# Kernel optimization log

Hardware: AMD Instinct MI355X
Metric: run time of the kernel (lower is better)

The kernel has to match this reference:

```python
import jax, jax.numpy as jnp
import numpy as np

B, N, D_IN, D_HID = 8, 2048, 512, 512

def setup_inputs() -> dict:
    key = jax.random.key(0)
    k1, k2, k3 = jax.random.split(key, 3)
    inp = jax.random.normal(k1, (B, N, D_IN), dtype=jnp.float32)
    # nn.Linear(input_size, hidden_size): weight [hidden, in], bias [hidden]
    W = jax.random.normal(k2, (D_HID, D_IN), dtype=jnp.float32) * (1.0 / np.sqrt(D_IN))
    b = jax.random.normal(k3, (D_HID,), dtype=jnp.float32) * 0.01
    return {"input": inp, "W": W, "b": b}

def reference(input, W, b):
    # x = fc(input): [B, N, D_HID]
    x = jnp.einsum('bnd,hd->bnh', input, W) + b
    # scores = x @ x^T (NO scale factor, matching the original): [B, N, N]
    scores = jnp.einsum('bnh,bmh->bnm', x, x)
    attn = jax.nn.softmax(scores, axis=2)
    # output = attn @ raw input (V = input, not the projection): [B, N, D_IN]
    output = jnp.einsum('bnm,bmd->bnd', attn, input)
    return output
```

## Files before the change

kernel.cpp:

```cpp
#include <hip/hip_runtime.h>
#include <hip/hip_bf16.h>
#include <stdint.h>

typedef short vbf16x8 __attribute__((ext_vector_type(8)));
typedef float vf32x4 __attribute__((ext_vector_type(4)));
typedef unsigned short u16;

__device__ __forceinline__ float bf2f(u16 u) {
  union { unsigned int i; float f; } v; v.i = ((unsigned int)u) << 16; return v.f;
}
__device__ __forceinline__ u16 f2bf(float f) {
  union { float f; unsigned int i; } v; v.f = f;
  return (u16)((v.i + 0x7fffu + ((v.i >> 16) & 1u)) >> 16);
}
__device__ __forceinline__ void gld16(const void* g, void* l) {
  __builtin_amdgcn_global_load_lds((const __attribute__((address_space(1))) void*)g,
                                   (__attribute__((address_space(3))) void*)l, 16, 0, 0);
}
template<int N> __device__ __forceinline__ void wait_vmcnt() {
  asm volatile("s_waitcnt vmcnt(%0)" :: "n"(N) : "memory");
}
__device__ __forceinline__ vbf16x8 ldsv(const u16* p) { return *(const vbf16x8*)p; }

__global__ __launch_bounds__(256) void k_convw(const float* __restrict__ W, u16* __restrict__ Wb) {
  int i = blockIdx.x * 256 + threadIdx.x;
  float4 x = ((const float4*)W)[i];
  ushort4 h;
  h.x = f2bf(x.x); h.y = f2bf(x.y); h.z = f2bf(x.z); h.w = f2bf(x.w);
  ((ushort4*)Wb)[i] = h;
}

__global__ __launch_bounds__(256) void k_prep(const float* __restrict__ in,
                                              u16* __restrict__ Abf, u16* __restrict__ Vt) {
  __shared__ u16 Ts[64][72];
  const int tid = threadIdx.x;
  const int n0 = blockIdx.x * 64, d0 = blockIdx.y * 64, b = blockIdx.z;
  const float* src = in + ((long long)b * 2048 + n0) * 512 + d0;
#pragma unroll
  for (int j = 0; j < 4; ++j) {
    int chunk = tid + 256 * j;
    int r = chunk >> 4, c = (chunk & 15) * 4;
    float4 x = *(const float4*)(src + (long long)r * 512 + c);
    ushort4 h;
    h.x = f2bf(x.x); h.y = f2bf(x.y); h.z = f2bf(x.z); h.w = f2bf(x.w);
    *(ushort4*)(Abf + ((long long)b * 2048 + n0 + r) * 512 + d0 + c) = h;
    Ts[c + 0][r] = h.x; Ts[c + 1][r] = h.y; Ts[c + 2][r] = h.z; Ts[c + 3][r] = h.w;
  }
  __syncthreads();
#pragma unroll
  for (int j = 0; j < 2; ++j) {
    int chunk = tid + 256 * j;
    int dr = chunk >> 3, c8 = (chunk & 7) * 8;
    vbf16x8 w = *(const vbf16x8*)&Ts[dr][c8];
    *(vbf16x8*)(Vt + ((long long)b * 512 + d0 + dr) * 2048 + n0 + c8) = w;
  }
}

__global__ __launch_bounds__(256) void k_rownorm(const u16* __restrict__ X,
                                                 float* __restrict__ D) {
  const int row = blockIdx.x * 4 + (threadIdx.x >> 6);
  const int lane = threadIdx.x & 63;
  vbf16x8 v = *(const vbf16x8*)(X + (long long)row * 512 + lane * 8);
  float s = 0.0f;
#pragma unroll
  for (int j = 0; j < 8; ++j) { float x = bf2f((u16)v[j]); s = fmaf(x, x, s); }
  for (int o = 1; o < 64; o <<= 1) s += __shfl_xor(s, o);
  if (lane == 0) D[row] = s;
}

__device__ __forceinline__ void sround(const u16* g, int K, int k0, u16* ldsbuf,
                                       int r, int srow, int scol, int wv) {
  gld16(g + (long long)(r * 64 + srow) * K + k0 + scol, ldsbuf + r * 4096 + wv * 512);
}

template<bool OUTBF, bool BIAS, int MAP, bool NORM>
__global__ __launch_bounds__(512, 2) void k_gemm(const u16* __restrict__ A,
                                                 const u16* __restrict__ Bt,
                                                 const float* __restrict__ bias,
                                                 void* __restrict__ Cout,
                                                 int M, int N, int K,
                                                 long long sA, long long sB, long long sC) {
  __shared__ __align__(16) u16 As[3 * 16384];
  __shared__ __align__(16) u16 Bs[3 * 8192];

  const int tid = threadIdx.x, lane = tid & 63, wv = tid >> 6;
  const int wr = wv >> 2, wc = wv & 3;

  const int lin = blockIdx.x;
  const int xcd = lin & 7, idx = lin >> 3;
  int zb, browi, bcoli;
  if constexpr (MAP == 1) { zb = 0; browi = xcd * 8 + (idx >> 2); bcoli = idx & 3; }
  else { zb = xcd; browi = idx >> 2; bcoli = idx & 3; }
  const int brow = browi * 256, bcol = bcoli * 128;
  const long long z = zb;

  const u16* gA = A + z * sA + (long long)brow * K;
  const u16* gB = Bt + z * sB + (long long)bcol * K;
  const int NT = K >> 6;

  const int srow = wv * 8 + (lane >> 3);
  const int scol = (((lane & 7) ^ ((lane >> 3) & 7)) << 3);
  const int rd0 = (lane & 15) * 64 + ((((lane >> 4)) ^ (lane & 7)) << 3);
  const int wrb = wr * 8192;
  const int wcb = wc * 2048;

  vf32x4 acc[8][2] = {};
  vf32x4 accl[8] = {};
  vbf16x8 afr[4], bfr[2];
  vbf16x8 ones;
  if constexpr (NORM) {
#pragma unroll
    for (int j = 0; j < 8; ++j) ones[j] = (short)0x3F80;
  }

  u16 *A0 = As, *A1 = As + 16384, *A2 = As + 32768;
  u16 *B0 = Bs, *B1 = Bs + 8192, *B2 = Bs + 16384;

  sround(gA, K, 0, A0, 0, srow, scol, wv);
  sround(gA, K, 0, A0, 1, srow, scol, wv);
  sround(gA, K, 0, A0, 2, srow, scol, wv);
  sround(gA, K, 0, A0, 3, srow, scol, wv);
  sround(gB, K, 0, B0, 0, srow, scol, wv);
  sround(gB, K, 0, B0, 1, srow, scol, wv);
  sround(gA, K, 64, A1, 0, srow, scol, wv);
  sround(gA, K, 64, A1, 1, srow, scol, wv);
  sround(gA, K, 64, A1, 2, srow, scol, wv);
  sround(gA, K, 64, A1, 3, srow, scol, wv);
  sround(gB, K, 64, B1, 0, srow, scol, wv);
  sround(gB, K, 64, B1, 1, srow, scol, wv);

  for (int t = 0; t < NT; ++t) {
    const int k2 = (t + 2) * 64;
    const bool st = (t + 2 < NT);

    if (t < NT - 1) wait_vmcnt<6>(); else wait_vmcnt<0>();
    __builtin_amdgcn_sched_barrier(0);
    __builtin_amdgcn_s_barrier();
    __builtin_amdgcn_sched_barrier(0);

#pragma unroll
    for (int n = 0; n < 2; ++n) bfr[n] = ldsv(B0 + wcb + n * 1024 + rd0);
#pragma unroll
    for (int i = 0; i < 4; ++i) afr[i] = ldsv(A0 + wrb + i * 1024 + rd0);
    if (st) { sround(gA, K, k2, A2, 0, srow, scol, wv); sround(gA, K, k2, A2, 1, srow, scol, wv); }
    __builtin_amdgcn_s_setprio(1);
#pragma unroll
    for (int i = 0; i < 4; ++i)
#pragma unroll
      for (int n = 0; n < 2; ++n)
        acc[i][n] = __builtin_amdgcn_mfma_f32_16x16x32_bf16(afr[i], bfr[n], acc[i][n], 0, 0, 0);
    if constexpr (NORM) {
#pragma unroll
      for (int i = 0; i < 4; ++i)
        accl[i] = __builtin_amdgcn_mfma_f32_16x16x32_bf16(afr[i], ones, accl[i], 0, 0, 0);
    }
    __builtin_amdgcn_s_setprio(0);

#pragma unroll
    for (int i = 0; i < 4; ++i) afr[i] = ldsv(A0 + wrb + (4 + i) * 1024 + rd0);
    if (st) sround(gA, K, k2, A2, 2, srow, scol, wv);
    __builtin_amdgcn_s_setprio(1);
#pragma unroll
    for (int i = 0; i < 4; ++i)
#pragma unroll
      for (int n = 0; n < 2; ++n)
        acc[4 + i][n] = __builtin_amdgcn_mfma_f32_16x16x32_bf16(afr[i], bfr[n], acc[4 + i][n], 0, 0, 0);
    if constexpr (NORM) {
#pragma unroll
      for (int i = 0; i < 4; ++i)
        accl[4 + i] = __builtin_amdgcn_mfma_f32_16x16x32_bf16(afr[i], ones, accl[4 + i], 0, 0, 0);
    }
    __builtin_amdgcn_s_setprio(0);

#pragma unroll
    for (int n = 0; n < 2; ++n) bfr[n] = ldsv(B0 + wcb + n * 1024 + (rd0 ^ 32));
#pragma unroll
    for (int i = 0; i < 4; ++i) afr[i] = ldsv(A0 + wrb + i * 1024 + (rd0 ^ 32));
    if (st) { sround(gA, K, k2, A2, 3, srow, scol, wv); sround(gB, K, k2, B2, 0, srow, scol, wv); }
    __builtin_amdgcn_s_setprio(1);
#pragma unroll
    for (int i = 0; i < 4; ++i)
#pragma unroll
      for (int n = 0; n < 2; ++n)
        acc[i][n] = __builtin_amdgcn_mfma_f32_16x16x32_bf16(afr[i], bfr[n], acc[i][n], 0, 0, 0);
    if constexpr (NORM) {
#pragma unroll
      for (int i = 0; i < 4; ++i)
        accl[i] = __builtin_amdgcn_mfma_f32_16x16x32_bf16(afr[i], ones, accl[i], 0, 0, 0);
    }
    __builtin_amdgcn_s_setprio(0);

#pragma unroll
    for (int i = 0; i < 4; ++i) afr[i] = ldsv(A0 + wrb + (4 + i) * 1024 + (rd0 ^ 32));
    if (st) sround(gB, K, k2, B2, 1, srow, scol, wv);
    __builtin_amdgcn_s_setprio(1);
#pragma unroll
    for (int i = 0; i < 4; ++i)
#pragma unroll
      for (int n = 0; n < 2; ++n)
        acc[4 + i][n] = __builtin_amdgcn_mfma_f32_16x16x32_bf16(afr[i], bfr[n], acc[4 + i][n], 0, 0, 0);
    if constexpr (NORM) {
#pragma unroll
      for (int i = 0; i < 4; ++i)
        accl[4 + i] = __builtin_amdgcn_mfma_f32_16x16x32_bf16(afr[i], ones, accl[4 + i], 0, 0, 0);
    }
    __builtin_amdgcn_s_setprio(0);

    u16* ta = A0; A0 = A1; A1 = A2; A2 = ta;
    u16* tb = B0; B0 = B1; B1 = B2; B2 = tb;
  }

  const long long zc = z * sC;
#pragma unroll
  for (int m = 0; m < 8; ++m) {
    const int row0 = brow + wr * 128 + m * 16 + (lane >> 4) * 4;
#pragma unroll
    for (int n = 0; n < 2; ++n) {
      const int col = bcol + wc * 32 + n * 16 + (lane & 15);
      const float bv = BIAS ? bias[col] : 0.0f;
#pragma unroll
      for (int r = 0; r < 4; ++r) {
        float v = acc[m][n][r] + bv;
        if constexpr (NORM) v = v / accl[m][r];
        const long long off = zc + (long long)(row0 + r) * N + col;
        if (OUTBF) ((u16*)Cout)[off] = f2bf(v);
        else       ((float*)Cout)[off] = v;
      }
    }
  }
}

__device__ __forceinline__ void sr32(const u16* g, int K, int k0, u16* ldsbuf,
                                     int r, int srow, int scol, int wv) {
  gld16(g + (long long)(r * 128 + srow) * K + k0 + scol, ldsbuf + r * 4096 + wv * 512);
}

__global__ __launch_bounds__(512, 2) void k_gemmS(const u16* __restrict__ X,
                                                  const float* __restrict__ D,
                                                  u16* __restrict__ P) {
  constexpr int K = 512, N = 2048;
  __shared__ __align__(16) u16 As[3 * 8192];
  __shared__ __align__(16) u16 Bs[3 * 8192];

  const int tid = threadIdx.x, lane = tid & 63, wv = tid >> 6;
  const int wr = wv >> 2, wc = wv & 3;

  const int lin = blockIdx.x;
  const int xcd = lin & 7, idx = lin >> 3;
  const int brow = (idx >> 3) * 256, bcol = (idx & 7) * 256;
  const long long z = xcd;

  const u16* gA = X + z * (2048LL * 512) + (long long)brow * K;
  const u16* gB = X + z * (2048LL * 512) + (long long)bcol * K;
  const int NT = K >> 5;

  const int srow = wv * 16 + (lane >> 2);
  const int scol = (((lane & 3) ^ ((lane >> 3) & 3)) << 3);
  const int rd = (lane & 15) * 32 + ((((lane >> 4)) ^ (((lane & 15) >> 1) & 3)) << 3);
  const int wrb = wr * 4096;
  const int wcb = wc * 2048;

  vf32x4 acc[8][4] = {};
  vbf16x8 afr[4], bfr[4];

  u16 *A0 = As, *A1 = As + 8192, *A2 = As + 16384;
  u16 *B0 = Bs, *B1 = Bs + 8192, *B2 = Bs + 16384;

  sr32(gA, K, 0, A0, 0, srow, scol, wv);
  sr32(gA, K, 0, A0, 1, srow, scol, wv);
  sr32(gB, K, 0, B0, 0, srow, scol, wv);
  sr32(gB, K, 0, B0, 1, srow, scol, wv);
  sr32(gA, K, 32, A1, 0, srow, scol, wv);
  sr32(gA, K, 32, A1, 1, srow, scol, wv);
  sr32(gB, K, 32, B1, 0, srow, scol, wv);
  sr32(gB, K, 32, B1, 1, srow, scol, wv);

  for (int t = 0; t < NT; ++t) {
    const int k2 = (t + 2) * 32;
    const bool st = (t + 2 < NT);

    if (t < NT - 1) wait_vmcnt<4>(); else wait_vmcnt<0>();
    __builtin_amdgcn_sched_barrier(0);
    __builtin_amdgcn_s_barrier();
    __builtin_amdgcn_sched_barrier(0);

#pragma unroll
    for (int n = 0; n < 4; ++n) bfr[n] = ldsv(B0 + wcb + n * 512 + rd);
#pragma unroll
    for (int i = 0; i < 4; ++i) afr[i] = ldsv(A0 + wrb + i * 512 + rd);
    if (st) { sr32(gA, K, k2, A2, 0, srow, scol, wv); sr32(gA, K, k2, A2, 1, srow, scol, wv); }
    __builtin_amdgcn_s_setprio(1);
#pragma unroll
    for (int i = 0; i < 4; ++i)
#pragma unroll
      for (int n = 0; n < 4; ++n)
        acc[i][n] = __builtin_amdgcn_mfma_f32_16x16x32_bf16(afr[i], bfr[n], acc[i][n], 0, 0, 0);
    __builtin_amdgcn_s_setprio(0);

#pragma unroll
    for (int i = 0; i < 4; ++i) afr[i] = ldsv(A0 + wrb + (4 + i) * 512 + rd);
    if (st) { sr32(gB, K, k2, B2, 0, srow, scol, wv); sr32(gB, K, k2, B2, 1, srow, scol, wv); }
    __builtin_amdgcn_s_setprio(1);
#pragma unroll
    for (int i = 0; i < 4; ++i)
#pragma unroll
      for (int n = 0; n < 4; ++n)
        acc[4 + i][n] = __builtin_amdgcn_mfma_f32_16x16x32_bf16(afr[i], bfr[n], acc[4 + i][n], 0, 0, 0);
    __builtin_amdgcn_s_setprio(0);

    u16* ta = A0; A0 = A1; A1 = A2; A2 = ta;
    u16* tb = B0; B0 = B1; B1 = B2; B2 = tb;
  }

  const float* Dz = D + z * 2048;
  const long long zc = z * (2048LL * 2048);
#pragma unroll
  for (int m = 0; m < 8; ++m) {
    const int row0 = brow + wr * 128 + m * 16 + (lane >> 4) * 4;
#pragma unroll
    for (int r = 0; r < 4; ++r) {
      const float dv = Dz[row0 + r];
#pragma unroll
      for (int n = 0; n < 4; ++n) {
        const int col = bcol + wc * 64 + n * 16 + (lane & 15);
        const float p = __expf(acc[m][n][r] - dv);
        P[zc + (long long)(row0 + r) * N + col] = f2bf(p);
      }
    }
  }
}

extern "C" void kernel_launch(void* const* d_in, const int* in_sizes, int n_in,
                              void* d_out, int out_size, void* d_ws, size_t ws_size,
                              hipStream_t stream) {
  const float* input = (const float*)d_in[0];
  const float* W     = (const float*)d_in[1];
  const float* bias  = (const float*)d_in[2];
  float* out = (float*)d_out;

  char* ws = (char*)d_ws;
  u16* Xbf = (u16*)(ws);
  u16* Vt  = (u16*)(ws + 16777216);
  u16* P   = (u16*)(ws + 2LL * 16777216);
  u16* Abf = (u16*)(ws + 2LL * 16777216);
  u16* Wb  = (u16*)(ws + 3LL * 16777216);
  float* D = out;

  k_convw<<<256, 256, 0, stream>>>(W, Wb);
  k_prep<<<dim3(32, 8, 8), 256, 0, stream>>>(input, Abf, Vt);
  k_gemm<true, true, 1, false><<<256, 512, 0, stream>>>(
      Abf, Wb, bias, Xbf, 16384, 512, 512, 0, 0, 0);
  k_rownorm<<<4096, 256, 0, stream>>>(Xbf, D);
  k_gemmS<<<512, 512, 0, stream>>>(Xbf, D, P);
  k_gemm<false, false, 2, true><<<256, 512, 0, stream>>>(
      P, Vt, nullptr, out, 2048, 512, 2048,
      2048LL * 2048, 512LL * 2048, 2048LL * 512);
}
```

Before: 115.8 us.

## Stage softmax P tiles through LDS for 16-byte stores; dedupe row-sum MFMAs

The score kernel's epilogue now writes exp'd bf16 values into an LDS staging tile and then emits coalesced 16-byte global stores, replacing scattered 2-byte stores to the large P matrix. In the normalizing GEMM, each wave now computes the ones-vector row-sum MFMAs only for its own share of rows, not every wave redundantly. The partial sums are shared through a small LDS array after a barrier. This adds several block barriers and LDS traffic in the epilogues, and the row-sum split relies on the wave-to-row mapping being correct.

After: 121.3 us. +4.8%, slower.

```diff
diff --git a/kernel.cpp b/kernel.cpp
--- a/kernel.cpp
+++ b/kernel.cpp
@@ -82,6 +82,7 @@
                                                  long long sA, long long sB, long long sC) {
   __shared__ __align__(16) u16 As[3 * 16384];
   __shared__ __align__(16) u16 Bs[3 * 8192];
+  __shared__ float Lsh[256];
 
   const int tid = threadIdx.x, lane = tid & 63, wv = tid >> 6;
   const int wr = wv >> 2, wc = wv & 3;
@@ -152,7 +153,8 @@
     if constexpr (NORM) {
 #pragma unroll
       for (int i = 0; i < 4; ++i)
-        accl[i] = __builtin_amdgcn_mfma_f32_16x16x32_bf16(afr[i], ones, accl[i], 0, 0, 0);
+        if ((i >> 1) == wc)
+          accl[i] = __builtin_amdgcn_mfma_f32_16x16x32_bf16(afr[i], ones, accl[i], 0, 0, 0);
     }
     __builtin_amdgcn_s_setprio(0);
 
@@ -168,7 +170,8 @@
     if constexpr (NORM) {
 #pragma unroll
       for (int i = 0; i < 4; ++i)
-        accl[4 + i] = __builtin_amdgcn_mfma_f32_16x16x32_bf16(afr[i], ones, accl[4 + i], 0, 0, 0);
+        if (2 + (i >> 1) == wc)
+          accl[4 + i] = __builtin_amdgcn_mfma_f32_16x16x32_bf16(afr[i], ones, accl[4 + i], 0, 0, 0);
     }
     __builtin_amdgcn_s_setprio(0);
 
@@ -186,7 +189,8 @@
     if constexpr (NORM) {
 #pragma unroll
       for (int i = 0; i < 4; ++i)
-        accl[i] = __builtin_amdgcn_mfma_f32_16x16x32_bf16(afr[i], ones, accl[i], 0, 0, 0);
+        if ((i >> 1) == wc)
+          accl[i] = __builtin_amdgcn_mfma_f32_16x16x32_bf16(afr[i], ones, accl[i], 0, 0, 0);
     }
     __builtin_amdgcn_s_setprio(0);
 
@@ -202,7 +206,8 @@
     if constexpr (NORM) {
 #pragma unroll
       for (int i = 0; i < 4; ++i)
-        accl[4 + i] = __builtin_amdgcn_mfma_f32_16x16x32_bf16(afr[i], ones, accl[4 + i], 0, 0, 0);
+        if (2 + (i >> 1) == wc)
+          accl[4 + i] = __builtin_amdgcn_mfma_f32_16x16x32_bf16(afr[i], ones, accl[4 + i], 0, 0, 0);
     }
     __builtin_amdgcn_s_setprio(0);
 
@@ -210,10 +215,24 @@
     u16* tb = B0; B0 = B1; B1 = B2; B2 = tb;
   }
 
+  if constexpr (NORM) {
+    if ((lane & 15) == 0) {
+#pragma unroll
+      for (int mm = 0; mm < 2; ++mm) {
+        const int m = wc * 2 + mm;
+#pragma unroll
+        for (int r = 0; r < 4; ++r)
+          Lsh[wr * 128 + m * 16 + (lane >> 4) * 4 + r] = accl[m][r];
+      }
+    }
+    __builtin_amdgcn_s_barrier();
+  }
+
   const long long zc = z * sC;
 #pragma unroll
   for (int m = 0; m < 8; ++m) {
-    const int row0 = brow + wr * 128 + m * 16 + (lane >> 4) * 4;
+    const int rloc = wr * 128 + m * 16 + (lane >> 4) * 4;
+    const int row0 = brow + rloc;
 #pragma unroll
     for (int n = 0; n < 2; ++n) {
       const int col = bcol + wc * 32 + n * 16 + (lane & 15);
@@ -221,7 +240,7 @@
 #pragma unroll
       for (int r = 0; r < 4; ++r) {
         float v = acc[m][n][r] + bv;
-        if constexpr (NORM) v = v / accl[m][r];
+        if constexpr (NORM) v = v / Lsh[rloc + r];
         const long long off = zc + (long long)(row0 + r) * N + col;
         if (OUTBF) ((u16*)Cout)[off] = f2bf(v);
         else       ((float*)Cout)[off] = v;
@@ -312,20 +331,35 @@
     u16* tb = B0; B0 = B1; B1 = B2; B2 = tb;
   }
 
+  __builtin_amdgcn_s_barrier();
+  u16* T = As;
   const float* Dz = D + z * 2048;
   const long long zc = z * (2048LL * 2048);
 #pragma unroll
-  for (int m = 0; m < 8; ++m) {
-    const int row0 = brow + wr * 128 + m * 16 + (lane >> 4) * 4;
-#pragma unroll
-    for (int r = 0; r < 4; ++r) {
-      const float dv = Dz[row0 + r];
-#pragma unroll
-      for (int n = 0; n < 4; ++n) {
-        const int col = bcol + wc * 64 + n * 16 + (lane & 15);
-        const float p = __expf(acc[m][n][r] - dv);
-        P[zc + (long long)(row0 + r) * N + col] = f2bf(p);
+  for (int m2 = 0; m2 < 4; ++m2) {
+    if (m2) __builtin_amdgcn_s_barrier();
+#pragma unroll
+    for (int mm = 0; mm < 2; ++mm) {
+      const int m = m2 * 2 + mm;
+      const int trow0 = wr * 32 + mm * 16 + (lane >> 4) * 4;
+#pragma unroll
+      for (int r = 0; r < 4; ++r) {
+        const float dv = Dz[brow + wr * 128 + m2 * 32 + mm * 16 + (lane >> 4) * 4 + r];
+#pragma unroll
+        for (int n = 0; n < 4; ++n) {
+          const float p = __expf(acc[m][n][r] - dv);
+          T[(trow0 + r) * 264 + wc * 64 + n * 16 + (lane & 15)] = f2bf(p);
+        }
       }
+    }
+    __builtin_amdgcn_s_barrier();
+#pragma unroll
+    for (int j = 0; j < 4; ++j) {
+      const int chunk = tid + 512 * j;
+      const int trow = chunk >> 5, c8 = (chunk & 31) * 8;
+      vbf16x8 w = *(const vbf16x8*)&T[trow * 264 + c8];
+      const int grow = brow + (trow >> 5) * 128 + m2 * 32 + (trow & 31);
+      *(vbf16x8*)&P[zc + (long long)grow * 2048 + bcol + c8] = w;
     }
   }
 }
```
